# Optimization experiments

Hardware: AMD Instinct MI355X
Metric: run time of the kernel (lower is better)

## Reference

```python
import jax, jax.numpy as jnp
import numpy as np

HEADS = 16
DIM_HEAD = 64
INNER = HEADS * DIM_HEAD  # 1024
QDIM = 1024
CDIM = 1024


def setup_inputs() -> dict:
    key = jax.random.key(0)
    ks = jax.random.split(key, 7)
    x = jax.random.normal(ks[0], (4, 2048, QDIM), dtype=jnp.float32)
    context = jax.random.normal(ks[1], (4, CDIM), dtype=jnp.float32)
    s = 0.02
    Wq = jax.random.normal(ks[2], (QDIM, INNER), dtype=jnp.float32) * s
    Wk = jax.random.normal(ks[3], (CDIM, INNER), dtype=jnp.float32) * s
    Wv = jax.random.normal(ks[4], (CDIM, INNER), dtype=jnp.float32) * s
    Wo = jax.random.normal(ks[5], (INNER, QDIM), dtype=jnp.float32) * s
    bo = jnp.zeros((QDIM,), dtype=jnp.float32)
    return {"x": x, "context": context, "Wq": Wq, "Wk": Wk, "Wv": Wv, "Wo": Wo, "bo": bo}


def reference(x, context, Wq, Wk, Wv, Wo, bo):
    B, N, _ = x.shape
    H, D = HEADS, DIM_HEAD
    scale = D ** (-0.5)
    # implicit cross attention: context (B, C) -> (B, 1, C)
    ctx = context[:, None, :]
    q = (x @ Wq).reshape(B, N, H, D).transpose(0, 2, 1, 3)      # (B,H,N,D)
    k = (ctx @ Wk).reshape(B, 1, H, D).transpose(0, 2, 1, 3)    # (B,H,1,D)
    v = (ctx @ Wv).reshape(B, 1, H, D).transpose(0, 2, 1, 3)
    # implicit cross-attn: prepend context token's k/v, append q as k/v
    k = jnp.concatenate([k, q], axis=2)  # (B,H,N+1,D)
    v = jnp.concatenate([v, q], axis=2)
    M = N + 1
    sim = jnp.einsum('bhid,bhjd->bhij', q, k) * scale  # (B,H,N,M)
    # causal mask with diagonal offset = k_len - q_len (implicit path)
    causal = jnp.tril(jnp.ones((N, M), dtype=bool), k=M - N)
    neg = -jnp.finfo(sim.dtype).max
    sim = jnp.where(causal[None, None], sim, neg)
    attn = jax.nn.softmax(sim, axis=-1)
    out = jnp.einsum('bhij,bhjd->bhid', attn, v)  # (B,H,N,D)
    out = out.transpose(0, 2, 1, 3).reshape(B, N, H * D)
    return out @ Wo + bo
```

## Files before the change

kernel.cpp:

```cpp
#include <hip/hip_runtime.h>
#include <stdint.h>

#define B_ 4
#define N_ 2048
#define H_ 16
#define D_ 64
#define QD 1024
#define SCALE 0.125f
#define LOG2E 1.44269504f
#define SC2 (SCALE * LOG2E)

typedef __bf16 bf16x8 __attribute__((ext_vector_type(8)));
typedef float f32x4 __attribute__((ext_vector_type(4)));
typedef float f32x16 __attribute__((ext_vector_type(16)));
typedef unsigned short u16x8 __attribute__((ext_vector_type(8)));
typedef unsigned short u16x4 __attribute__((ext_vector_type(4)));
typedef unsigned short ushort_t;

__device__ __forceinline__ unsigned short f2bf(float f) {
  union { float f; unsigned u; } x; x.f = f;
  unsigned r = (x.u + 0x7fffu + ((x.u >> 16) & 1u)) >> 16;
  return (unsigned short)r;
}

__device__ __forceinline__ void ldg2lds16(const void* g, void* l) {
  __builtin_amdgcn_global_load_lds(
      (const __attribute__((address_space(1))) void*)g,
      (__attribute__((address_space(3))) void*)l, 16, 0, 0);
}

__device__ __forceinline__ ushort_t bfbits(float f) {
  union { __bf16 b; ushort_t u; } x; x.b = (__bf16)f; return x.u;
}

__global__ __launch_bounds__(256) void k_prep(const float* __restrict__ x,
    ushort_t* __restrict__ xb, const float* __restrict__ Wq,
    const float* __restrict__ Wo, ushort_t* __restrict__ WqT,
    ushort_t* __restrict__ WoT, const float* __restrict__ ctx,
    const float* __restrict__ Wk, const float* __restrict__ Wv,
    float* __restrict__ part) {
  __shared__ __align__(16) char arena[64 * 65 * 4];
  const int wg = blockIdx.x;
  const int t = threadIdx.x;
  if (wg < 4096) {
    int i = wg * 256 + t;
    const float4* p = (const float4*)x + (size_t)i * 2;
    float4 a = p[0], b = p[1];
    u16x8 r;
    r[0] = f2bf(a.x); r[1] = f2bf(a.y); r[2] = f2bf(a.z); r[3] = f2bf(a.w);
    r[4] = f2bf(b.x); r[5] = f2bf(b.y); r[6] = f2bf(b.z); r[7] = f2bf(b.w);
    *((u16x8*)xb + i) = r;
  } else if (wg < 4608) {
    const int wgl = wg - 4096;
    const float* W = (wgl >> 8) ? Wo : Wq;
    ushort_t* WT = (wgl >> 8) ? WoT : WqT;
    float (*tile)[65] = (float(*)[65])arena;
    int n0 = (wgl & 15) * 64, k0 = ((wgl >> 4) & 15) * 64;
    int tx = t & 63, ty = t >> 6;
#pragma unroll
    for (int i = 0; i < 64; i += 4)
      tile[ty + i][tx] = W[(size_t)(k0 + ty + i) * QD + n0 + tx];
    __syncthreads();
#pragma unroll
    for (int i = 0; i < 64; i += 4)
      WT[(size_t)(n0 + ty + i) * QD + k0 + tx] = f2bf(tile[tx][ty + i]);
  } else {
    const int wgl = wg - 4608;
    const int ich = wgl & 3, ks = (wgl >> 2) & 7, kv = wgl >> 5;
    const float* W = kv ? Wv : Wk;
    float (*cs)[128] = (float(*)[128])arena;
    for (int i = t; i < B_ * 128; i += 256)
      cs[i >> 7][i & 127] = ctx[(size_t)(i >> 7) * QD + ks * 128 + (i & 127)];
    __syncthreads();
    int col = ich * 256 + t;
    float a0 = 0, a1 = 0, a2 = 0, a3 = 0;
    for (int k = 0; k < 128; k++) {
      float w = W[(size_t)(ks * 128 + k) * QD + col];
      a0 += cs[0][k] * w; a1 += cs[1][k] * w; a2 += cs[2][k] * w; a3 += cs[3][k] * w;
    }
    float* p = part + (size_t)(ks * 2 + kv) * (B_ * QD);
    p[0 * QD + col] = a0; p[1 * QD + col] = a1; p[2 * QD + col] = a2; p[3 * QD + col] = a3;
  }
}

__global__ __launch_bounds__(256) void k_ctx_reduce(const float* __restrict__ part,
    float* __restrict__ kctx, float* __restrict__ vctx) {
  int idx = blockIdx.x * 256 + threadIdx.x;
  int kv = idx >> 12;
  int rest = idx & 4095;
  float acc = 0;
  for (int ks = 0; ks < 8; ks++) acc += part[(size_t)(ks * 2 + kv) * 4096 + rest];
  (kv ? vctx : kctx)[rest] = acc;
}

template <int BF16OUT, int WRITEQT>
__global__ __launch_bounds__(256) void k_gemm(const ushort_t* __restrict__ A,
    const ushort_t* __restrict__ Bm, ushort_t* __restrict__ Cb, float* __restrict__ Cf,
    const float* __restrict__ bias, ushort_t* __restrict__ qT) {
  __shared__ __align__(16) char arena[WRITEQT ? (128 * 136 * 2) : (128 * 64 * 2 * 2)];
  ushort_t* As = (ushort_t*)arena;
  ushort_t* Bs = (ushort_t*)arena + 128 * 64;
  const int wg = blockIdx.x;
  const int by = (wg & 7) * 8 + ((wg >> 3) & 7);
  const int bx = wg >> 6;
  const int t = threadIdx.x;
  const int w = t >> 6, l = t & 63;
  const int wr = w >> 1, wc = w & 1;
  const int lr = l & 15, lg = l >> 4;
  const int m0 = by * 128, n0 = bx * 128;
  f32x4 acc[4][4] = {};
  for (int k0 = 0; k0 < QD; k0 += 64) {
#pragma unroll
    for (int rep = 0; rep < 4; rep++) {
      int c = t + rep * 256;
      int row = c >> 3, c0 = 8 * ((c & 7) ^ (row & 7));
      ldg2lds16(&A[(size_t)(m0 + row) * QD + k0 + c0], &As[c * 8]);
      ldg2lds16(&Bm[(size_t)(n0 + row) * QD + k0 + c0], &Bs[c * 8]);
    }
    __syncthreads();
#pragma unroll
    for (int kk = 0; kk < 2; kk++) {
      bf16x8 af[4], bfr[4];
#pragma unroll
      for (int m = 0; m < 4; m++) {
        int row = wr * 64 + m * 16 + lr;
        af[m] = *(const bf16x8*)((const char*)As + row * 128 +
                                 (((kk * 4 + lg) ^ (row & 7)) << 4));
      }
#pragma unroll
      for (int n = 0; n < 4; n++) {
        int row = wc * 64 + n * 16 + lr;
        bfr[n] = *(const bf16x8*)((const char*)Bs + row * 128 +
                                  (((kk * 4 + lg) ^ (row & 7)) << 4));
      }
#pragma unroll
      for (int m = 0; m < 4; m++)
#pragma unroll
        for (int n = 0; n < 4; n++)
          acc[m][n] = __builtin_amdgcn_mfma_f32_16x16x32_bf16(af[m], bfr[n], acc[m][n], 0, 0, 0);
    }
    __syncthreads();
  }
#pragma unroll
  for (int m = 0; m < 4; m++) {
    int row = m0 + wr * 64 + m * 16 + lg * 4;
#pragma unroll
    for (int n = 0; n < 4; n++) {
      int col = n0 + wc * 64 + n * 16 + lr;
#pragma unroll
      for (int j = 0; j < 4; j++) {
        float v = acc[m][n][j];
        if constexpr (BF16OUT) {
          Cb[(size_t)(row + j) * QD + col] = f2bf(v);
        } else {
          Cf[(size_t)(row + j) * QD + col] = v + bias[col];
        }
      }
    }
  }
  if constexpr (WRITEQT) {
    ushort_t* T2 = (ushort_t*)arena;
#pragma unroll
    for (int m = 0; m < 4; m++) {
      int rowl = wr * 64 + m * 16 + lg * 4;
#pragma unroll
      for (int n = 0; n < 4; n++) {
        int col = wc * 64 + n * 16 + lr;
        u16x4 v;
#pragma unroll
        for (int j = 0; j < 4; j++) v[j] = f2bf(acc[m][n][j]);
        *(u16x4*)&T2[col * 136 + rowl] = v;
      }
    }
    __syncthreads();
    const int c = t & 127, r0 = (t >> 7) * 64;
    const int h = (n0 + c) >> 6, d = (n0 + c) & 63;
    const int b = m0 >> 11, nloc = (m0 & 2047) + r0;
    ushort_t* dst = qT + ((size_t)(b * 16 + h) * 64 + d) * (size_t)N_ + nloc;
#pragma unroll
    for (int i = 0; i < 8; i++)
      *(u16x8*)(dst + i * 8) = *(const u16x8*)&T2[c * 136 + r0 + i * 8];
  }
}

__global__ __launch_bounds__(512, 4) void k_attn14(
    const ushort_t* __restrict__ q, const ushort_t* __restrict__ qT,
    const float* __restrict__ kctx, const float* __restrict__ vctx,
    ushort_t* __restrict__ att) {
  const int wg = blockIdx.x;
  const int k8 = wg >> 6;
  const int s = (k8 < 4) ? k8 : (11 - k8);
  const int bh = ((wg & 7) << 3) | ((wg >> 3) & 7);
  const int b = bh >> 4, h = bh & 15;
  const int t = threadIdx.x, w = t >> 6, l = t & 63;
  const int lq = l & 31, hi = l >> 5;
  const int wq0 = s * 256 + w * 32;

  __shared__ __align__(128) ushort_t Ks[2][2][4096];
  __shared__ __align__(128) ushort_t Vs[2][2][4096];

  const ushort_t* qbase = q + (size_t)b * N_ * QD + h * D_;
  const ushort_t* qtb = qT + (size_t)bh * D_ * N_;
  const float* kc = kctx + bh * D_;
  const float* vc = vctx + bh * D_;

  const int srow = t >> 3;
  const int scol = 8 * ((t & 7) ^ ((t >> 3) & 7));

  const int NI = 2 * s + 2;

  const ushort_t* stK = qbase + (size_t)srow * QD + scol;
  const ushort_t* stV = qtb + (size_t)srow * N_ + scol;

  auto stage = [&](int pr, int j) {
    ldg2lds16(stK, &Ks[pr][j][t * 8]);
    ldg2lds16(stV, &Vs[pr][j][t * 8]);
    stK += (size_t)64 * QD;
    stV += 64;
  };

  stage(0, 0);
  stage(0, 1);

  bf16x8 qf[4];
#pragma unroll
  for (int kk = 0; kk < 4; kk++) {
    qf[kk] = *(const bf16x8*)&qbase[(size_t)(wq0 + lq) * QD + kk * 16 + hi * 8];
#pragma unroll
    for (int j = 0; j < 8; j++)
      qf[kk][j] = (__bf16)((float)qf[kk][j] * SC2);
  }

  float ew, lacc;
  f32x16 oacc[2];
  {
    float dot = 0.f;
#pragma unroll
    for (int kk = 0; kk < 4; kk++)
#pragma unroll
      for (int j = 0; j < 8; j++)
        dot += (float)qf[kk][j] * kc[kk * 16 + hi * 8 + j];
    dot += __shfl_xor(dot, 32);
    ew = __builtin_exp2f(dot);
    lacc = 0.0f;
#pragma unroll
    for (int dt = 0; dt < 2; dt++)
#pragma unroll
      for (int r = 0; r < 16; r++)
        oacc[dt][r] = vc[dt * 32 + (r & 3) + 8 * (r >> 2) + 4 * hi] * ew;
  }

  auto body = [&](int tt, const char* ksb, const char* vsb) {
    const int j0 = tt * 64;
    if (j0 > wq0 + 31) return;

    f32x16 p[2];
    __builtin_amdgcn_s_setprio(1);
#pragma unroll
    for (int kb = 0; kb < 2; kb++) {
      f32x16 acc = {};
#pragma unroll
      for (int kk = 0; kk < 4; kk++) {
        bf16x8 kf = *(const bf16x8*)(ksb + (l & 31) * 128 + kb * 4096 +
                                     (((kk * 2 + hi) ^ (l & 7)) << 4));
        acc = __builtin_amdgcn_mfma_f32_32x32x16_bf16(kf, qf[kk], acc, 0, 0, 0);
      }
      p[kb] = acc;
    }
    __builtin_amdgcn_s_setprio(0);

    if (j0 + 63 > wq0) {
      const int qrel = wq0 - j0 + lq;
#pragma unroll
      for (int kb = 0; kb < 2; kb++)
#pragma unroll
        for (int r = 0; r < 16; r++) {
          int key = kb * 32 + (r & 3) + 8 * (r >> 2) + 4 * hi;
          if (key > qrel) p[kb][r] = -1e30f;
        }
    }

#pragma unroll
    for (int kb = 0; kb < 2; kb++)
#pragma unroll
      for (int r = 0; r < 16; r++)
        p[kb][r] = __builtin_exp2f(p[kb][r]);
    float s8[8];
#pragma unroll
    for (int r = 0; r < 8; r++)
      s8[r] = (p[0][r] + p[0][r + 8]) + (p[1][r] + p[1][r + 8]);
    float s4a = s8[0] + s8[4], s4b = s8[1] + s8[5];
    float s4c = s8[2] + s8[6], s4d = s8[3] + s8[7];
    lacc += (s4a + s4b) + (s4c + s4d);

#pragma unroll
    for (int kb = 0; kb < 2; kb++) {
      unsigned u[8];
#pragma unroll
      for (int i = 0; i < 8; i++) {
        float lo = p[kb][2 * i], hi2 = p[kb][2 * i + 1];
        asm("v_cvt_pk_bf16_f32 %0, %1, %2" : "=v"(u[i]) : "v"(lo), "v"(hi2));
      }
      asm("v_permlane32_swap_b32 %0, %1" : "+v"(u[0]), "+v"(u[2]));
      asm("v_permlane32_swap_b32 %0, %1" : "+v"(u[1]), "+v"(u[3]));
      asm("v_permlane32_swap_b32 %0, %1" : "+v"(u[4]), "+v"(u[6]));
      asm("v_permlane32_swap_b32 %0, %1" : "+v"(u[5]), "+v"(u[7]));
      union { unsigned u4[4]; bf16x8 v; } pf0, pf1;
      pf0.u4[0] = u[0]; pf0.u4[1] = u[1]; pf0.u4[2] = u[2]; pf0.u4[3] = u[3];
      pf1.u4[0] = u[4]; pf1.u4[1] = u[5]; pf1.u4[2] = u[6]; pf1.u4[3] = u[7];
      __builtin_amdgcn_s_setprio(1);
#pragma unroll
      for (int ks = 0; ks < 2; ks++) {
        const bf16x8 pf = ks ? pf1.v : pf0.v;
#pragma unroll
        for (int dt = 0; dt < 2; dt++) {
          bf16x8 vf = *(const bf16x8*)(vsb + (l & 31) * 128 + dt * 4096 +
                                       (((kb * 4 + ks * 2 + hi) ^ (l & 7)) << 4));
          oacc[dt] = __builtin_amdgcn_mfma_f32_32x32x16_bf16(vf, pf, oacc[dt], 0, 0, 0);
        }
      }
      __builtin_amdgcn_s_setprio(0);
    }
  };

  for (int it = 0; it < NI; ++it) {
    const int pr = it & 1;
    if (it + 1 < NI) {
      stage(pr ^ 1, 0);
      stage(pr ^ 1, 1);
      asm volatile("s_waitcnt vmcnt(4)" ::: "memory");
    } else {
      asm volatile("s_waitcnt vmcnt(0)" ::: "memory");
    }
    __builtin_amdgcn_s_barrier();

    body(2 * it,     (const char*)&Ks[pr][0][0], (const char*)&Vs[pr][0][0]);
    body(2 * it + 1, (const char*)&Ks[pr][1][0], (const char*)&Vs[pr][1][0]);

    __builtin_amdgcn_s_barrier();
  }

  const float lsum = ew + lacc + __shfl_xor(lacc, 32);
  const float inv = 1.0f / lsum;
  ushort_t* ob = att + (size_t)b * N_ * QD + (size_t)(wq0 + lq) * QD + h * D_;
#pragma unroll
  for (int dt = 0; dt < 2; dt++)
#pragma unroll
    for (int rq = 0; rq < 4; rq++) {
      union { ushort_t s4[4]; unsigned long long v; } o;
#pragma unroll
      for (int e = 0; e < 4; e++) o.s4[e] = bfbits(oacc[dt][rq * 4 + e] * inv);
      *(unsigned long long*)(ob + dt * 32 + 8 * rq + 4 * hi) = o.v;
    }
}

extern "C" void kernel_launch(void* const* d_in, const int* in_sizes, int n_in,
                              void* d_out, int out_size, void* d_ws, size_t ws_size,
                              hipStream_t stream) {
  const float* x = (const float*)d_in[0];
  const float* ctx = (const float*)d_in[1];
  const float* Wq = (const float*)d_in[2];
  const float* Wk = (const float*)d_in[3];
  const float* Wv = (const float*)d_in[4];
  const float* Wo = (const float*)d_in[5];
  const float* bo = (const float*)d_in[6];
  float* out = (float*)d_out;

  char* ws = (char*)d_ws;
  size_t off = 0;
  ushort_t* xb = (ushort_t*)(ws + off);   off += (size_t)8192 * 1024 * 2;
  ushort_t* qb = (ushort_t*)(ws + off);   off += (size_t)8192 * 1024 * 2;
  ushort_t* attb = (ushort_t*)(ws + off); off += (size_t)8192 * 1024 * 2;
  ushort_t* WqT = (ushort_t*)(ws + off);  off += (size_t)1024 * 1024 * 2;
  ushort_t* WoT = (ushort_t*)(ws + off);  off += (size_t)1024 * 1024 * 2;
  float* kctx = (float*)(ws + off);       off += (size_t)4096 * 4;
  float* vctx = (float*)(ws + off);       off += (size_t)4096 * 4;
  float* part = (float*)(ws + off);       off += (size_t)16 * 4096 * 4;
  ushort_t* qT2 = (ushort_t*)(ws + off);  off += (size_t)8192 * 1024 * 2;

  k_prep<<<dim3(4672), dim3(256), 0, stream>>>(x, xb, Wq, Wo, WqT, WoT,
                                               ctx, Wk, Wv, part);
  k_ctx_reduce<<<dim3(32), dim3(256), 0, stream>>>(part, kctx, vctx);
  k_gemm<1, 1><<<dim3(512), dim3(256), 0, stream>>>(xb, WqT, qb, nullptr, nullptr, qT2);
  k_attn14<<<dim3(512), dim3(512), 0, stream>>>(qb, qT2, kctx, vctx, attb);
  k_gemm<0, 0><<<dim3(512), dim3(256), 0, stream>>>(attb, WoT, nullptr, out, bo, nullptr);
}
```

Baseline: 139.7 us.

## Fuse x fp32-to-bf16 conversion into Q GEMM and drop split-K context reduce

The separate pass that converted x to bf16 is removed. The Q projection GEMM now loads fp32 x directly, converts it in registers and stores bf16 into LDS, which avoids writing and re-reading a 16MB intermediate. The context K/V projection now runs a full-K loop per block instead of split-K partials, so the separate reduce kernel and one launch go away. The trade-off is that the A operand load in the GEMM becomes synchronous through registers instead of an async global-to-LDS copy, and the context projection has much less parallelism with only 8 blocks each looping over K=1024.

```diff
diff --git a/kernel.cpp b/kernel.cpp
--- a/kernel.cpp
+++ b/kernel.cpp
@@ -33,29 +33,19 @@
   union { __bf16 b; ushort_t u; } x; x.b = (__bf16)f; return x.u;
 }
 
-__global__ __launch_bounds__(256) void k_prep(const float* __restrict__ x,
-    ushort_t* __restrict__ xb, const float* __restrict__ Wq,
+__global__ __launch_bounds__(256) void k_prep(const float* __restrict__ Wq,
     const float* __restrict__ Wo, ushort_t* __restrict__ WqT,
     ushort_t* __restrict__ WoT, const float* __restrict__ ctx,
     const float* __restrict__ Wk, const float* __restrict__ Wv,
-    float* __restrict__ part) {
-  __shared__ __align__(16) char arena[64 * 65 * 4];
+    float* __restrict__ kctx, float* __restrict__ vctx) {
+  __shared__ __align__(16) float arena[4 * QD];
   const int wg = blockIdx.x;
   const int t = threadIdx.x;
-  if (wg < 4096) {
-    int i = wg * 256 + t;
-    const float4* p = (const float4*)x + (size_t)i * 2;
-    float4 a = p[0], b = p[1];
-    u16x8 r;
-    r[0] = f2bf(a.x); r[1] = f2bf(a.y); r[2] = f2bf(a.z); r[3] = f2bf(a.w);
-    r[4] = f2bf(b.x); r[5] = f2bf(b.y); r[6] = f2bf(b.z); r[7] = f2bf(b.w);
-    *((u16x8*)xb + i) = r;
-  } else if (wg < 4608) {
-    const int wgl = wg - 4096;
-    const float* W = (wgl >> 8) ? Wo : Wq;
-    ushort_t* WT = (wgl >> 8) ? WoT : WqT;
+  if (wg < 512) {
+    const float* W = (wg >> 8) ? Wo : Wq;
+    ushort_t* WT = (wg >> 8) ? WoT : WqT;
     float (*tile)[65] = (float(*)[65])arena;
-    int n0 = (wgl & 15) * 64, k0 = ((wgl >> 4) & 15) * 64;
+    int n0 = (wg & 15) * 64, k0 = ((wg >> 4) & 15) * 64;
     int tx = t & 63, ty = t >> 6;
 #pragma unroll
     for (int i = 0; i < 64; i += 4)
@@ -65,36 +55,31 @@
     for (int i = 0; i < 64; i += 4)
       WT[(size_t)(n0 + ty + i) * QD + k0 + tx] = f2bf(tile[tx][ty + i]);
   } else {
-    const int wgl = wg - 4608;
-    const int ich = wgl & 3, ks = (wgl >> 2) & 7, kv = wgl >> 5;
+    const int g = wg - 512;
+    const int kv = g >> 2, cc = g & 3;
     const float* W = kv ? Wv : Wk;
-    float (*cs)[128] = (float(*)[128])arena;
-    for (int i = t; i < B_ * 128; i += 256)
-      cs[i >> 7][i & 127] = ctx[(size_t)(i >> 7) * QD + ks * 128 + (i & 127)];
-    __syncthreads();
-    int col = ich * 256 + t;
+    float* dst = kv ? vctx : kctx;
+    for (int i = t; i < 4 * QD; i += 256) arena[i] = ctx[i];
+    __syncthreads();
+    const int col = cc * 256 + t;
     float a0 = 0, a1 = 0, a2 = 0, a3 = 0;
-    for (int k = 0; k < 128; k++) {
-      float w = W[(size_t)(ks * 128 + k) * QD + col];
-      a0 += cs[0][k] * w; a1 += cs[1][k] * w; a2 += cs[2][k] * w; a3 += cs[3][k] * w;
-    }
-    float* p = part + (size_t)(ks * 2 + kv) * (B_ * QD);
-    p[0 * QD + col] = a0; p[1 * QD + col] = a1; p[2 * QD + col] = a2; p[3 * QD + col] = a3;
-  }
-}
-
-__global__ __launch_bounds__(256) void k_ctx_reduce(const float* __restrict__ part,
-    float* __restrict__ kctx, float* __restrict__ vctx) {
-  int idx = blockIdx.x * 256 + threadIdx.x;
-  int kv = idx >> 12;
-  int rest = idx & 4095;
-  float acc = 0;
-  for (int ks = 0; ks < 8; ks++) acc += part[(size_t)(ks * 2 + kv) * 4096 + rest];
-  (kv ? vctx : kctx)[rest] = acc;
-}
-
-template <int BF16OUT, int WRITEQT>
-__global__ __launch_bounds__(256) void k_gemm(const ushort_t* __restrict__ A,
+#pragma unroll 4
+    for (int k = 0; k < QD; k++) {
+      float w = W[(size_t)k * QD + col];
+      a0 += arena[0 * QD + k] * w;
+      a1 += arena[1 * QD + k] * w;
+      a2 += arena[2 * QD + k] * w;
+      a3 += arena[3 * QD + k] * w;
+    }
+    dst[0 * QD + col] = a0;
+    dst[1 * QD + col] = a1;
+    dst[2 * QD + col] = a2;
+    dst[3 * QD + col] = a3;
+  }
+}
+
+template <int BF16OUT, int WRITEQT, int A_FP32>
+__global__ __launch_bounds__(256) void k_gemm(const void* __restrict__ Av,
     const ushort_t* __restrict__ Bm, ushort_t* __restrict__ Cb, float* __restrict__ Cf,
     const float* __restrict__ bias, ushort_t* __restrict__ qT) {
   __shared__ __align__(16) char arena[WRITEQT ? (128 * 136 * 2) : (128 * 64 * 2 * 2)];
@@ -108,13 +93,24 @@
   const int wr = w >> 1, wc = w & 1;
   const int lr = l & 15, lg = l >> 4;
   const int m0 = by * 128, n0 = bx * 128;
+  const ushort_t* Ab = (const ushort_t*)Av;
+  const float* Af = (const float*)Av;
   f32x4 acc[4][4] = {};
   for (int k0 = 0; k0 < QD; k0 += 64) {
 #pragma unroll
     for (int rep = 0; rep < 4; rep++) {
       int c = t + rep * 256;
       int row = c >> 3, c0 = 8 * ((c & 7) ^ (row & 7));
-      ldg2lds16(&A[(size_t)(m0 + row) * QD + k0 + c0], &As[c * 8]);
+      if constexpr (A_FP32) {
+        const float* src = &Af[(size_t)(m0 + row) * QD + k0 + c0];
+        float4 f0 = *(const float4*)src, f1 = *(const float4*)(src + 4);
+        u16x8 v;
+        v[0] = f2bf(f0.x); v[1] = f2bf(f0.y); v[2] = f2bf(f0.z); v[3] = f2bf(f0.w);
+        v[4] = f2bf(f1.x); v[5] = f2bf(f1.y); v[6] = f2bf(f1.z); v[7] = f2bf(f1.w);
+        *(u16x8*)&As[c * 8] = v;
+      } else {
+        ldg2lds16(&Ab[(size_t)(m0 + row) * QD + k0 + c0], &As[c * 8]);
+      }
       ldg2lds16(&Bm[(size_t)(n0 + row) * QD + k0 + c0], &Bs[c * 8]);
     }
     __syncthreads();
@@ -368,20 +364,17 @@
 
   char* ws = (char*)d_ws;
   size_t off = 0;
-  ushort_t* xb = (ushort_t*)(ws + off);   off += (size_t)8192 * 1024 * 2;
   ushort_t* qb = (ushort_t*)(ws + off);   off += (size_t)8192 * 1024 * 2;
   ushort_t* attb = (ushort_t*)(ws + off); off += (size_t)8192 * 1024 * 2;
   ushort_t* WqT = (ushort_t*)(ws + off);  off += (size_t)1024 * 1024 * 2;
   ushort_t* WoT = (ushort_t*)(ws + off);  off += (size_t)1024 * 1024 * 2;
   float* kctx = (float*)(ws + off);       off += (size_t)4096 * 4;
   float* vctx = (float*)(ws + off);       off += (size_t)4096 * 4;
-  float* part = (float*)(ws + off);       off += (size_t)16 * 4096 * 4;
   ushort_t* qT2 = (ushort_t*)(ws + off);  off += (size_t)8192 * 1024 * 2;
 
-  k_prep<<<dim3(4672), dim3(256), 0, stream>>>(x, xb, Wq, Wo, WqT, WoT,
-                                               ctx, Wk, Wv, part);
-  k_ctx_reduce<<<dim3(32), dim3(256), 0, stream>>>(part, kctx, vctx);
-  k_gemm<1, 1><<<dim3(512), dim3(256), 0, stream>>>(xb, WqT, qb, nullptr, nullptr, qT2);
+  k_prep<<<dim3(520), dim3(256), 0, stream>>>(Wq, Wo, WqT, WoT, ctx, Wk, Wv,
+                                              kctx, vctx);
+  k_gemm<1, 1, 1><<<dim3(512), dim3(256), 0, stream>>>(x, WqT, qb, nullptr, nullptr, qT2);
   k_attn14<<<dim3(512), dim3(512), 0, stream>>>(qb, qT2, kctx, vctx, attb);
-  k_gemm<0, 0><<<dim3(512), dim3(256), 0, stream>>>(attb, WoT, nullptr, out, bo, nullptr);
-}
+  k_gemm<0, 0, 0><<<dim3(512), dim3(256), 0, stream>>>(attb, WoT, nullptr, out, bo, nullptr);
+}
```

Measured after the change: 219.7 us. 1.57x slower.
